# Kernel optimization log

Measured on AMD Instinct MI355X. Metric: run time of the kernel, lower is better.

Reference implementation:

```python
import jax, jax.numpy as jnp
import numpy as np

NHEAD = 8

def layernorm(x, w, b, eps=1e-5):
    mu = jnp.mean(x, axis=-1, keepdims=True)
    var = jnp.mean((x - mu) ** 2, axis=-1, keepdims=True)
    return (x - mu) * jax.lax.rsqrt(var + eps) * w + b

def setup_inputs() -> dict:
    key = jax.random.key(0)
    ks = jax.random.split(key, 3)
    N, in_dim, dim = 2048, 256, 256
    point = jax.random.normal(ks[0], (N, in_dim), dtype=jnp.float32)
    w_qkv = jax.random.normal(ks[1], (in_dim, 3 * dim), dtype=jnp.float32) * (in_dim ** -0.5)
    w_proj = jax.random.normal(ks[2], (dim, dim), dtype=jnp.float32) * (dim ** -0.5)
    return {
        "point": point,
        "w_qkv": w_qkv,
        "w_proj": w_proj,
        "b_proj": jnp.zeros((dim,), jnp.float32),
        "norm1_w": jnp.ones((in_dim,), jnp.float32),
        "norm1_b": jnp.zeros((in_dim,), jnp.float32),
        "norm2_w": jnp.ones((dim,), jnp.float32),
        "norm2_b": jnp.zeros((dim,), jnp.float32),
        "topk": 16,
    }

def reference(point, w_qkv, w_proj, b_proj, norm1_w, norm1_b, norm2_w, norm2_b, topk):
    # Coarse level of QTAttB (i == 0, ONE_BATCH=True)
    N, in_dim = point.shape
    dim = w_proj.shape[0]
    Ch = dim // NHEAD  # per-head channels
    x = layernorm(point, norm1_w, norm1_b)[None]            # [1, N, in_dim]
    qkv = (x @ w_qkv).reshape(1, N, 3, NHEAD, Ch)
    q, k, v = qkv[:, :, 0], qkv[:, :, 1], qkv[:, :, 2]      # [1, N, H, Ch]
    # QK: nlhd,nshd->nlsh ; softmax over key axis s (dim=-2 in torch = axis 2)
    QK = jnp.einsum('blhd,bshd->blsh', q, k)                # [1, N, N, H]
    A = jax.nn.softmax(QK * (Ch ** -0.5), axis=2)
    A_mean = jnp.mean(A, axis=-1)                           # [1, N, N]
    _, topk_idx = jax.lax.top_k(A_mean, topk)               # [1, N, topk]
    message = jnp.einsum('blsh,bshd->blhd', A, v).reshape(1, N, dim)
    message = message @ w_proj + b_proj
    message = v.reshape(1, N, dim) + message
    message = message[0]                                    # squeeze batch
    out = layernorm(message, norm2_w, norm2_b)              # final_message = norm2(message)
    return out, topk_idx[0]
```

## Files before the change

### kernel.cpp

```cpp
#include <hip/hip_runtime.h>

#define NTOK   2048
#define DIM    256
#define NH     8
#define CH     32
#define QB     8
#define TOPK_K 16
#define SCALE  0.17677669529663687f
#define LN_EPS 1e-5f

#define PBL    260
#define PBH    (QB * PBL)
#define PSCALE 16384.f
#define RPSCALE (1.f / 16384.f)

typedef _Float16 h16;
typedef _Float16 h16x8 __attribute__((ext_vector_type(8)));
typedef float    f32x4 __attribute__((ext_vector_type(4)));

#define MFMA16(a, b, c) __builtin_amdgcn_mfma_f32_16x16x32_f16((a), (b), (c), 0, 0, 0)


template<int NT>
__device__ __forceinline__ float block_sum(float v, float* red){
  #pragma unroll
  for (int off = 32; off > 0; off >>= 1) v += __shfl_xor(v, off, 64);
  const int t = threadIdx.x;
  if ((t & 63) == 0) red[t >> 6] = v;
  __syncthreads();
  float s = 0.f;
  #pragma unroll
  for (int w = 0; w < NT/64; w++) s += red[w];
  __syncthreads();
  return s;
}

__global__ __launch_bounds__(256) void reorder_w_kernel(
    const float* __restrict__ src_qkv, const float* __restrict__ src_proj,
    h16* __restrict__ WF, h16* __restrict__ WP)
{
  const int b = blockIdx.x;
  const float* src; h16* dst; int ld, pair;
  if (b < 96){ src = src_qkv;  dst = WF; ld = 768; pair = b * 4 + (threadIdx.x >> 6); }
  else       { src = src_proj; dst = WP; ld = 256; pair = (b - 96) * 4 + (threadIdx.x >> 6); }
  const int l  = threadIdx.x & 63;
  const int cg = pair >> 3, ks = pair & 7;
  h16x8 hi8, lo8;
  #pragma unroll
  for (int j = 0; j < 8; j++){
    const float v = src[(size_t)(ks * 32 + (l >> 4) * 8 + j) * ld + cg * 16 + (l & 15)];
    const h16 h = (h16)v;
    hi8[j] = h;
    lo8[j] = (h16)(v - (float)h);
  }
  *(h16x8*)&dst[(size_t)((cg * 8 + ks) * 2 + 0) * 512 + l * 8] = hi8;
  *(h16x8*)&dst[(size_t)((cg * 8 + ks) * 2 + 1) * 512 + l * 8] = lo8;
}

__global__ __launch_bounds__(1024) void ln_qkv_kernel(
    const float* __restrict__ point,
    const h16*   __restrict__ WF,
    const float* __restrict__ c1,
    const float* __restrict__ c2,
    float* __restrict__ Q,
    h16*   __restrict__ KF,
    h16*   __restrict__ VF,
    float* __restrict__ V)
{
  __shared__ float xs[16][261];
  __shared__ float garr[256], barr[256];
  __shared__ float red[16];
  const int t  = threadIdx.x;
  const int wv = t >> 6;
  const int l  = t & 63;
  const int r  = l & 15;
  const int g  = l >> 4;
  const int tg = blockIdx.x >> 1;
  const int ch = blockIdx.x & 1;
  const int l0 = tg * 16;

  const float a1 = (t < 256) ? c1[t] : 0.f;
  const float a2 = (t < 256) ? c2[t] : 0.f;
  const float s1 = block_sum<1024>(fabsf(a1), red);
  const float s2 = block_sum<1024>(fabsf(a2), red);
  if (t < 256){ garr[t] = (s1 > s2) ? a1 : a2; barr[t] = (s1 > s2) ? a2 : a1; }
  __syncthreads();

  {
    const float4 x = *(const float4*)&point[(size_t)(l0 + wv) * DIM + 4 * l];
    float s = x.x + x.y + x.z + x.w;
    #pragma unroll
    for (int off = 1; off < 64; off <<= 1) s += __shfl_xor(s, off, 64);
    const float mu = s * (1.f / DIM);
    const float d0 = x.x - mu, d1 = x.y - mu, d2 = x.z - mu, d3 = x.w - mu;
    float ss = d0 * d0 + d1 * d1 + d2 * d2 + d3 * d3;
    #pragma unroll
    for (int off = 1; off < 64; off <<= 1) ss += __shfl_xor(ss, off, 64);
    const float rsd = rsqrtf(ss * (1.f / DIM) + LN_EPS);
    xs[wv][4 * l + 0] = d0 * rsd * garr[4 * l + 0] + barr[4 * l + 0];
    xs[wv][4 * l + 1] = d1 * rsd * garr[4 * l + 1] + barr[4 * l + 1];
    xs[wv][4 * l + 2] = d2 * rsd * garr[4 * l + 2] + barr[4 * l + 2];
    xs[wv][4 * l + 3] = d3 * rsd * garr[4 * l + 3] + barr[4 * l + 3];
  }
  __syncthreads();

  h16x8 ah[8], al[8];
  #pragma unroll
  for (int ks = 0; ks < 8; ks++){
    #pragma unroll
    for (int j = 0; j < 8; j++){
      const float v = xs[r][ks * 32 + 8 * g + j];
      const h16 hi = (h16)v;
      ah[ks][j] = hi;
      al[ks][j] = (h16)(v - (float)hi);
    }
  }

  const int kgb = tg;
  #pragma unroll
  for (int cgi = 0; cgi < 2; cgi++){
    if (cgi == 1 && wv >= 8) break;
    const int cg = ch * 24 + (cgi == 0 ? wv : 16 + wv);
    f32x4 acc = {0.f, 0.f, 0.f, 0.f};
    const h16* wf = WF + (size_t)cg * 8192 + (size_t)l * 8;
    #pragma unroll
    for (int ks = 0; ks < 8; ks++){
      const h16x8 bh = *(const h16x8*)(wf + ks * 1024);
      const h16x8 bl = *(const h16x8*)(wf + ks * 1024 + 512);
      acc = MFMA16(ah[ks], bh, acc);
      acc = MFMA16(al[ks], bh, acc);
      acc = MFMA16(ah[ks], bl, acc);
    }
    const int typ = cg >> 4;
    const int c0  = (cg & 15) * 16 + r;
    #pragma unroll
    for (int q4 = 0; q4 < 4; q4++){
      const int tok = 4 * g + q4;
      if (typ == 0){
        Q[(size_t)(l0 + tok) * DIM + c0] = acc[q4];
      } else if (typ == 1){
        const int wh = c0 >> 5, gp = (c0 & 31) >> 3, jj = c0 & 7;
        const float kv = acc[q4];
        const h16 kh2 = (h16)kv;
        const size_t kidx = (size_t)(wh * 128 + kgb) * 1024
                          + (size_t)(gp * 16 + tok) * 8 + jj;
        KF[kidx]       = kh2;
        KF[kidx + 512] = (h16)(kv - (float)kh2);
      } else {
        V[(size_t)(l0 + tok) * DIM + c0] = acc[q4];
        const int wh = c0 >> 5, hh = (c0 & 31) >> 4, cp = c0 & 15;
        const int key = l0 + tok;
        const int kb = key >> 5, krem = key & 31, gpp = krem >> 3, jpp = krem & 7;
        VF[(size_t)((wh * 64 + kb) * 2 + hh) * 512
           + (size_t)(gpp * 16 + cp) * 8 + jpp] = (h16)acc[q4];
      }
    }
  }
}

__global__ __launch_bounds__(1024) void z_kernel(
    const float* __restrict__ Q,
    const h16*   __restrict__ KF,
    float*       __restrict__ Zp)
{
  const int t  = threadIdx.x;
  const int wv = t >> 6;
  const int w  = wv & 7;
  const int sh = wv >> 3;
  const int l  = t & 63;
  const int r  = l & 15;
  const int g  = l >> 4;
  const int tg = blockIdx.x >> 1;
  const int hb = blockIdx.x & 1;

  h16x8 qh, ql;
  {
    const float* qp = &Q[(size_t)(tg * 16 + r) * DIM + w * CH + 8 * g];
    const float4 q0 = *(const float4*)qp;
    const float4 q1 = *(const float4*)(qp + 4);
    const float qv[8] = {q0.x, q0.y, q0.z, q0.w, q1.x, q1.y, q1.z, q1.w};
    #pragma unroll
    for (int j = 0; j < 8; j++){
      const float s = qv[j] * SCALE;
      const h16 hi = (h16)s;
      qh[j] = hi;
      ql[j] = (h16)(s - (float)hi);
    }
  }

  const h16* kf = KF + (size_t)(w * 128 + hb * 64 + sh * 32) * 1024 + (size_t)l * 8;
  float zs[4] = {0.f, 0.f, 0.f, 0.f};
  #pragma unroll 2
  for (int kgi = 0; kgi < 32; kgi++){
    const h16x8 bh = *(const h16x8*)(kf + (size_t)kgi * 1024);
    const h16x8 bl = *(const h16x8*)(kf + (size_t)kgi * 1024 + 512);
    f32x4 d = {0.f, 0.f, 0.f, 0.f};
    d = MFMA16(qh, bh, d);
    d = MFMA16(ql, bh, d);
    d = MFMA16(qh, bl, d);
    #pragma unroll
    for (int q4 = 0; q4 < 4; q4++) zs[q4] += __expf(d[q4]);
  }
  #pragma unroll
  for (int q4 = 0; q4 < 4; q4++){
    #pragma unroll
    for (int off = 1; off < 16; off <<= 1) zs[q4] += __shfl_xor(zs[q4], off, 64);
  }
  if (r == 0){
    #pragma unroll
    for (int q4 = 0; q4 < 4; q4++)
      Zp[(size_t)((hb * 2 + sh) * NH + w) * NTOK + tg * 16 + 4 * g + q4] = zs[q4];
  }
}

__global__ __launch_bounds__(1024) __attribute__((amdgpu_waves_per_eu(4)))
void attn_fused_kernel(
    const float* Q,
    const h16*   __restrict__ KF,
    const h16*   __restrict__ VF,
    const float* __restrict__ Zp,
    float*       msg,
    float*       __restrict__ out_idx)
{
  __shared__ float pbuf[NH * PBH];
  __shared__ float am[QB][NTOK];
  __shared__ float msg_s[2][QB][DIM + 4];
  __shared__ float zbuf[NH * QB];

  const int t  = threadIdx.x;
  const int wv = t >> 6;
  const int w  = wv & 7;
  const int hf = wv >> 3;
  const int l  = t & 63;
  const int r  = l & 15;
  const int g  = l >> 4;
  const int l0 = blockIdx.x * QB;

  h16x8 qh, ql;
  #pragma unroll
  for (int j = 0; j < 8; j++){ qh[j] = (h16)0.f; ql[j] = (h16)0.f; }
  if (r < QB){
    const float* qp = &Q[(size_t)(l0 + r) * DIM + w * CH + 8 * g];
    const float4 q0 = *(const float4*)qp;
    const float4 q1 = *(const float4*)(qp + 4);
    const float qv[8] = {q0.x, q0.y, q0.z, q0.w, q1.x, q1.y, q1.z, q1.w};
    #pragma unroll
    for (int j = 0; j < 8; j++){
      const float s = qv[j] * SCALE;
      const h16 hi = (h16)s;
      qh[j] = hi;
      ql[j] = (h16)(s - (float)hi);
    }
  }

  if (t < 64){
    const int h = t >> 3, q = t & 7;
    float z = 0.f;
    #pragma unroll
    for (int p = 0; p < 4; p++) z += Zp[(size_t)(p * NH + h) * NTOK + l0 + q];
    zbuf[t] = z;
  }
  __syncthreads();
  float rZ[4];
  #pragma unroll
  for (int q4 = 0; q4 < 4; q4++){
    const int row = 4 * g + q4;
    rZ[q4] = (g < 2) ? 1.f / zbuf[w * QB + row] : 0.f;
  }

  const h16* kfw = KF + (size_t)(w * 128) * 1024 + (size_t)l * 8;
  const h16* vfw = VF + (size_t)(w * 64) * 1024 + (size_t)l * 8;

  f32x4 macc[2];
  #pragma unroll
  for (int dg = 0; dg < 2; dg++) macc[dg] = (f32x4){0.f, 0.f, 0.f, 0.f};

  for (int ti = 0; ti < 8; ti++){
    const int s0 = ti * 256;
    const h16* vft = vfw + (size_t)((ti * 8 + hf * 4) * 2) * 512;

    h16x8 pva[4], pvb[4];
    pva[0] = *(const h16x8*)(vft);
    pvb[0] = *(const h16x8*)(vft + 512);
    pva[1] = *(const h16x8*)(vft + 1024);
    pvb[1] = *(const h16x8*)(vft + 1024 + 512);

    {
      const h16* kft = kfw + (size_t)(ti * 16 + hf * 8) * 1024;
      #pragma unroll 2
      for (int kgi = 0; kgi < 8; kgi++){
        const h16x8 bh = *(const h16x8*)(kft + (size_t)kgi * 1024);
        const h16x8 bl = *(const h16x8*)(kft + (size_t)kgi * 1024 + 512);
        f32x4 d = {0.f, 0.f, 0.f, 0.f};
        d = MFMA16(qh, bh, d);
        d = MFMA16(ql, bh, d);
        d = MFMA16(qh, bl, d);
        if (g < 2){
          const int kbr = hf * 128 + kgi * 16 + r;
          pbuf[w * PBH + (4 * g + 0) * PBL + kbr] = __expf(d[0]) * rZ[0];
          pbuf[w * PBH + (4 * g + 1) * PBL + kbr] = __expf(d[1]) * rZ[1];
          pbuf[w * PBH + (4 * g + 2) * PBL + kbr] = __expf(d[2]) * rZ[2];
          pbuf[w * PBH + (4 * g + 3) * PBL + kbr] = __expf(d[3]) * rZ[3];
        }
      }
    }
    __syncthreads();

    pva[2] = *(const h16x8*)(vft + 2048);
    pvb[2] = *(const h16x8*)(vft + 2048 + 512);
    pva[3] = *(const h16x8*)(vft + 3072);
    pvb[3] = *(const h16x8*)(vft + 3072 + 512);

    #pragma unroll
    for (int st = 0; st < 4; st++){
      h16x8 pa;
      #pragma unroll
      for (int j = 0; j < 8; j++) pa[j] = (h16)0.f;
      if (r < QB){
        const float* pp = &pbuf[w * PBH + r * PBL + hf * 128 + st * 32 + 8 * g];
        const float4 p0 = *(const float4*)pp;
        const float4 p1 = *(const float4*)(pp + 4);
        pa[0] = (h16)(p0.x * PSCALE); pa[1] = (h16)(p0.y * PSCALE);
        pa[2] = (h16)(p0.z * PSCALE); pa[3] = (h16)(p0.w * PSCALE);
        pa[4] = (h16)(p1.x * PSCALE); pa[5] = (h16)(p1.y * PSCALE);
        pa[6] = (h16)(p1.z * PSCALE); pa[7] = (h16)(p1.w * PSCALE);
      }
      macc[0] = MFMA16(pa, pva[st], macc[0]);
      macc[1] = MFMA16(pa, pvb[st], macc[1]);
    }
    if (t < 512){
      const int q = t >> 6, k4 = (t & 63) * 4;
      float4 su = make_float4(0.f, 0.f, 0.f, 0.f);
      #pragma unroll
      for (int hh = 0; hh < 8; hh++){
        const float4 v = *(const float4*)&pbuf[hh * PBH + q * PBL + k4];
        su.x += v.x; su.y += v.y; su.z += v.z; su.w += v.w;
      }
      *(float4*)&am[q][s0 + k4] =
          make_float4(su.x * 0.125f, su.y * 0.125f, su.z * 0.125f, su.w * 0.125f);
    }
    __syncthreads();
  }

  if (g < 2){
    #pragma unroll
    for (int dg = 0; dg < 2; dg++)
      #pragma unroll
      for (int q4 = 0; q4 < 4; q4++)
        msg_s[hf][4 * g + q4][w * CH + dg * 16 + r] = macc[dg][q4] * RPSCALE;
  }
  __syncthreads();

  if (wv < QB){
    for (int it = 0; it < TOPK_K; it++){
      float bv = -1e30f; int bi = 0x7fffffff;
      #pragma unroll
      for (int b = 0; b < NTOK / 64; b++){
        const int idx = b * 64 + l;
        const float v = am[wv][idx];
        if (v > bv || (v == bv && idx < bi)){ bv = v; bi = idx; }
      }
      #pragma unroll
      for (int off = 1; off < 64; off <<= 1){
        const float ov = __shfl_xor(bv, off, 64);
        const int   oi = __shfl_xor(bi, off, 64);
        if (ov > bv || (ov == bv && oi < bi)){ bv = ov; bi = oi; }
      }
      if (l == 0){
        out_idx[(l0 + wv) * TOPK_K + it] = (float)bi;
        am[wv][bi] = -1e30f;
      }
    }
  } else {
    const int t2 = t - 512;
    #pragma unroll
    for (int k2 = 0; k2 < 4; k2++){
      const int cell = t2 + 512 * k2;
      const int q = cell >> 8, dcol = cell & 255;
      msg[(size_t)(l0 + q) * DIM + dcol] = msg_s[0][q][dcol] + msg_s[1][q][dcol];
    }
  }
}

__global__ __launch_bounds__(1024) void proj_ln_kernel(
    const float* __restrict__ msg,
    const float* __restrict__ V,
    const h16*   __restrict__ WP,
    const float* __restrict__ b_proj,
    const float* __restrict__ c1,
    const float* __restrict__ c2,
    float* __restrict__ out)
{
  __shared__ float xs[16][261];
  __shared__ float ms2[16][261];
  __shared__ float garr[256], barr[256], bparr[256];
  __shared__ float red[16];
  const int t  = threadIdx.x;
  const int wv = t >> 6;
  const int l  = t & 63;
  const int r  = l & 15;
  const int g  = l >> 4;
  const int l0 = blockIdx.x * 16;

  const float a1 = (t < 256) ? c1[t] : 0.f;
  const float a2 = (t < 256) ? c2[t] : 0.f;
  const float s1 = block_sum<1024>(fabsf(a1), red);
  const float s2 = block_sum<1024>(fabsf(a2), red);
  if (t < 256){
    garr[t]  = (s1 > s2) ? a1 : a2;
    barr[t]  = (s1 > s2) ? a2 : a1;
    bparr[t] = b_proj[t];
  }

  {
    const float4 x = *(const float4*)&msg[(size_t)(l0 + wv) * DIM + 4 * l];
    xs[wv][4 * l + 0] = x.x; xs[wv][4 * l + 1] = x.y;
    xs[wv][4 * l + 2] = x.z; xs[wv][4 * l + 3] = x.w;
  }
  __syncthreads();

  h16x8 ah[8], al[8];
  #pragma unroll
  for (int ks = 0; ks < 8; ks++){
    #pragma unroll
    for (int j = 0; j < 8; j++){
      const float v = xs[r][ks * 32 + 8 * g + j];
      const h16 hi = (h16)v;
      ah[ks][j] = hi;
      al[ks][j] = (h16)(v - (float)hi);
    }
  }

  f32x4 acc = {0.f, 0.f, 0.f, 0.f};
  {
    const h16* wp = WP + (size_t)wv * 8192 + (size_t)l * 8;
    #pragma unroll
    for (int ks = 0; ks < 8; ks++){
      const h16x8 bh = *(const h16x8*)(wp + ks * 1024);
      const h16x8 bl = *(const h16x8*)(wp + ks * 1024 + 512);
      acc = MFMA16(ah[ks], bh, acc);
      acc = MFMA16(al[ks], bh, acc);
      acc = MFMA16(ah[ks], bl, acc);
    }
  }

  const int dc = wv * 16 + r;
  #pragma unroll
  for (int q4 = 0; q4 < 4; q4++){
    const int tok = 4 * g + q4;
    ms2[tok][dc] = acc[q4] + bparr[dc] + V[(size_t)(l0 + tok) * DIM + dc];
  }
  __syncthreads();

  {
    const float x0 = ms2[wv][4 * l + 0], x1 = ms2[wv][4 * l + 1];
    const float x2 = ms2[wv][4 * l + 2], x3 = ms2[wv][4 * l + 3];
    float s = x0 + x1 + x2 + x3;
    #pragma unroll
    for (int off = 1; off < 64; off <<= 1) s += __shfl_xor(s, off, 64);
    const float mu = s * (1.f / DIM);
    const float d0 = x0 - mu, d1 = x1 - mu, d2 = x2 - mu, d3 = x3 - mu;
    float ss = d0 * d0 + d1 * d1 + d2 * d2 + d3 * d3;
    #pragma unroll
    for (int off = 1; off < 64; off <<= 1) ss += __shfl_xor(ss, off, 64);
    const float rsd = rsqrtf(ss * (1.f / DIM) + LN_EPS);
    float4 o;
    o.x = d0 * rsd * garr[4 * l + 0] + barr[4 * l + 0];
    o.y = d1 * rsd * garr[4 * l + 1] + barr[4 * l + 1];
    o.z = d2 * rsd * garr[4 * l + 2] + barr[4 * l + 2];
    o.w = d3 * rsd * garr[4 * l + 3] + barr[4 * l + 3];
    *(float4*)&out[(size_t)(l0 + wv) * DIM + 4 * l] = o;
  }
}

extern "C" void kernel_launch(void* const* d_in, const int* in_sizes, int n_in,
                              void* d_out, int out_size, void* d_ws, size_t ws_size,
                              hipStream_t stream) {
  const float* point  = nullptr;
  const float* w_qkv  = nullptr;
  const float* w_proj = nullptr;
  const float* v256[5] = {nullptr, nullptr, nullptr, nullptr, nullptr};
  int n256 = 0;
  for (int i = 0; i < n_in; i++){
    const int sz = in_sizes[i];
    if      (sz == NTOK * DIM)      point  = (const float*)d_in[i];
    else if (sz == DIM * 3 * DIM)   w_qkv  = (const float*)d_in[i];
    else if (sz == DIM * DIM)       w_proj = (const float*)d_in[i];
    else if (sz == DIM && n256 < 5) v256[n256++] = (const float*)d_in[i];
  }
  const float* b_proj = v256[0];
  const float* n1a    = v256[1];
  const float* n1c    = v256[2];
  const float* n2a    = v256[3];
  const float* n2c    = v256[4];

  float* out     = (float*)d_out;
  float* out_idx = out + (size_t)NTOK * DIM;

  char* ws = (char*)d_ws;
  float* Q   = (float*)(ws);
  float* V   = (float*)(ws + ((size_t)2 << 20));
  h16*   KF  = (h16*)  (ws + ((size_t)4 << 20));
  h16*   VF  = (h16*)  (ws + ((size_t)6 << 20));
  h16*   WF  = (h16*)  (ws + ((size_t)7 << 20));
  h16*   WP  = (h16*)  (ws + ((size_t)7 << 20) + 786432);
  float* msg = Q;
  float* Zp  = out;

  reorder_w_kernel <<<128,       256,  0, stream>>>(w_qkv, w_proj, WF, WP);
  ln_qkv_kernel    <<<256,       1024, 0, stream>>>(point, WF, n1a, n1c, Q, KF, VF, V);
  z_kernel         <<<256,       1024, 0, stream>>>(Q, KF, Zp);
  attn_fused_kernel<<<NTOK / QB, 1024, 0, stream>>>(Q, KF, VF, Zp, msg, out_idx);
  proj_ln_kernel   <<<NTOK / 16, 1024, 0, stream>>>(msg, V, WP, b_proj, n2a, n2c, out);
}
```

Before: 181.0 us.

## Split attention keys across two blocks with full 16-row query tiles and two-stage top-k

The query tile grows from 8 to 16 rows, so the MFMA rows that were previously zero-padded now do real work. Each block handles one half of the keys. Partial messages are combined with atomicAdd into the output buffer, and each half writes 16 top-k candidates that a new topk_kernel merges. Q is stored once as prescaled fp16 hi/lo fragments instead of being converted from fp32 in both the z and attention kernels. The z partial sums are now accumulated with atomics too. This adds a zeroing kernel, an extra launch, atomic traffic and a reuse of workspace buffers.

```diff
diff --git a/kernel.cpp b/kernel.cpp
--- a/kernel.cpp
+++ b/kernel.cpp
@@ -4,7 +4,7 @@
 #define DIM    256
 #define NH     8
 #define CH     32
-#define QB     8
+#define QB     16
 #define TOPK_K 16
 #define SCALE  0.17677669529663687f
 #define LN_EPS 1e-5f
@@ -57,12 +57,20 @@
   *(h16x8*)&dst[(size_t)((cg * 8 + ks) * 2 + 1) * 512 + l * 8] = lo8;
 }
 
+__global__ __launch_bounds__(256) void zero2_kernel(
+    float* __restrict__ a, int na, float* __restrict__ b, int nb)
+{
+  const int stride = gridDim.x * blockDim.x;
+  for (int k = blockIdx.x * blockDim.x + threadIdx.x; k < na; k += stride) a[k] = 0.f;
+  for (int k = blockIdx.x * blockDim.x + threadIdx.x; k < nb; k += stride) b[k] = 0.f;
+}
+
 __global__ __launch_bounds__(1024) void ln_qkv_kernel(
     const float* __restrict__ point,
     const h16*   __restrict__ WF,
     const float* __restrict__ c1,
     const float* __restrict__ c2,
-    float* __restrict__ Q,
+    h16*   __restrict__ QF,
     h16*   __restrict__ KF,
     h16*   __restrict__ VF,
     float* __restrict__ V)
@@ -137,7 +145,12 @@
     for (int q4 = 0; q4 < 4; q4++){
       const int tok = 4 * g + q4;
       if (typ == 0){
-        Q[(size_t)(l0 + tok) * DIM + c0] = acc[q4];
+        const float qs = acc[q4] * SCALE;
+        const h16 qhi = (h16)qs;
+        const int wq = c0 >> 5, gq = (c0 & 31) >> 3, jq = c0 & 7;
+        const size_t qidx = (((size_t)(tg * 8 + wq) * 2 + 0) * 64 + (gq * 16 + tok)) * 8 + jq;
+        QF[qidx]       = qhi;
+        QF[qidx + 512] = (h16)(qs - (float)qhi);
       } else if (typ == 1){
         const int wh = c0 >> 5, gp = (c0 & 31) >> 3, jj = c0 & 7;
         const float kv = acc[q4];
@@ -159,9 +172,9 @@
 }
 
 __global__ __launch_bounds__(1024) void z_kernel(
-    const float* __restrict__ Q,
-    const h16*   __restrict__ KF,
-    float*       __restrict__ Zp)
+    const h16* __restrict__ QF,
+    const h16* __restrict__ KF,
+    float*     __restrict__ Zp)
 {
   const int t  = threadIdx.x;
   const int wv = t >> 6;
@@ -173,20 +186,9 @@
   const int tg = blockIdx.x >> 1;
   const int hb = blockIdx.x & 1;
 
-  h16x8 qh, ql;
-  {
-    const float* qp = &Q[(size_t)(tg * 16 + r) * DIM + w * CH + 8 * g];
-    const float4 q0 = *(const float4*)qp;
-    const float4 q1 = *(const float4*)(qp + 4);
-    const float qv[8] = {q0.x, q0.y, q0.z, q0.w, q1.x, q1.y, q1.z, q1.w};
-    #pragma unroll
-    for (int j = 0; j < 8; j++){
-      const float s = qv[j] * SCALE;
-      const h16 hi = (h16)s;
-      qh[j] = hi;
-      ql[j] = (h16)(s - (float)hi);
-    }
-  }
+  const h16* qf = QF + ((size_t)(tg * 8 + w) * 2) * 512 + (size_t)l * 8;
+  const h16x8 qh = *(const h16x8*)(qf);
+  const h16x8 ql = *(const h16x8*)(qf + 512);
 
   const h16* kf = KF + (size_t)(w * 128 + hb * 64 + sh * 32) * 1024 + (size_t)l * 8;
   float zs[4] = {0.f, 0.f, 0.f, 0.f};
@@ -209,23 +211,23 @@
   if (r == 0){
     #pragma unroll
     for (int q4 = 0; q4 < 4; q4++)
-      Zp[(size_t)((hb * 2 + sh) * NH + w) * NTOK + tg * 16 + 4 * g + q4] = zs[q4];
+      atomicAdd(&Zp[(size_t)w * NTOK + tg * 16 + 4 * g + q4], zs[q4]);
   }
 }
 
 __global__ __launch_bounds__(1024) __attribute__((amdgpu_waves_per_eu(4)))
 void attn_fused_kernel(
-    const float* Q,
+    const h16*   __restrict__ QF,
     const h16*   __restrict__ KF,
     const h16*   __restrict__ VF,
     const float* __restrict__ Zp,
-    float*       msg,
-    float*       __restrict__ out_idx)
+    float*       __restrict__ msgacc,
+    float2*      __restrict__ candG)
 {
   __shared__ float pbuf[NH * PBH];
-  __shared__ float am[QB][NTOK];
-  __shared__ float msg_s[2][QB][DIM + 4];
-  __shared__ float zbuf[NH * QB];
+  __shared__ float cand_v[16][64];
+  __shared__ float cand_i[16][64];
+  __shared__ float zbuf[NH][QB];
 
   const int t  = threadIdx.x;
   const int wv = t >> 6;
@@ -234,49 +236,28 @@
   const int l  = t & 63;
   const int r  = l & 15;
   const int g  = l >> 4;
-  const int l0 = blockIdx.x * QB;
-
-  h16x8 qh, ql;
-  #pragma unroll
-  for (int j = 0; j < 8; j++){ qh[j] = (h16)0.f; ql[j] = (h16)0.f; }
-  if (r < QB){
-    const float* qp = &Q[(size_t)(l0 + r) * DIM + w * CH + 8 * g];
-    const float4 q0 = *(const float4*)qp;
-    const float4 q1 = *(const float4*)(qp + 4);
-    const float qv[8] = {q0.x, q0.y, q0.z, q0.w, q1.x, q1.y, q1.z, q1.w};
-    #pragma unroll
-    for (int j = 0; j < 8; j++){
-      const float s = qv[j] * SCALE;
-      const h16 hi = (h16)s;
-      qh[j] = hi;
-      ql[j] = (h16)(s - (float)hi);
-    }
-  }
-
-  if (t < 64){
-    const int h = t >> 3, q = t & 7;
-    float z = 0.f;
-    #pragma unroll
-    for (int p = 0; p < 4; p++) z += Zp[(size_t)(p * NH + h) * NTOK + l0 + q];
-    zbuf[t] = z;
-  }
+  const int qt = blockIdx.x >> 1;
+  const int hb = blockIdx.x & 1;
+  const int l0 = qt * 16;
+
+  const h16* qf = QF + ((size_t)(qt * 8 + w) * 2) * 512 + (size_t)l * 8;
+  const h16x8 qh = *(const h16x8*)(qf);
+  const h16x8 ql = *(const h16x8*)(qf + 512);
+
+  if (t < 128) zbuf[t >> 4][t & 15] = Zp[(size_t)(t >> 4) * NTOK + l0 + (t & 15)];
   __syncthreads();
   float rZ[4];
   #pragma unroll
-  for (int q4 = 0; q4 < 4; q4++){
-    const int row = 4 * g + q4;
-    rZ[q4] = (g < 2) ? 1.f / zbuf[w * QB + row] : 0.f;
-  }
-
-  const h16* kfw = KF + (size_t)(w * 128) * 1024 + (size_t)l * 8;
-  const h16* vfw = VF + (size_t)(w * 64) * 1024 + (size_t)l * 8;
+  for (int q4 = 0; q4 < 4; q4++) rZ[q4] = 1.f / zbuf[w][4 * g + q4];
+
+  const h16* kfw = KF + (size_t)(w * 128 + hb * 64) * 1024 + (size_t)l * 8;
+  const h16* vfw = VF + (size_t)(w * 64 + hb * 32) * 1024 + (size_t)l * 8;
 
   f32x4 macc[2];
   #pragma unroll
   for (int dg = 0; dg < 2; dg++) macc[dg] = (f32x4){0.f, 0.f, 0.f, 0.f};
 
-  for (int ti = 0; ti < 8; ti++){
-    const int s0 = ti * 256;
+  for (int ti = 0; ti < 4; ti++){
     const h16* vft = vfw + (size_t)((ti * 8 + hf * 4) * 2) * 512;
 
     h16x8 pva[4], pvb[4];
@@ -295,13 +276,11 @@
         d = MFMA16(qh, bh, d);
         d = MFMA16(ql, bh, d);
         d = MFMA16(qh, bl, d);
-        if (g < 2){
-          const int kbr = hf * 128 + kgi * 16 + r;
-          pbuf[w * PBH + (4 * g + 0) * PBL + kbr] = __expf(d[0]) * rZ[0];
-          pbuf[w * PBH + (4 * g + 1) * PBL + kbr] = __expf(d[1]) * rZ[1];
-          pbuf[w * PBH + (4 * g + 2) * PBL + kbr] = __expf(d[2]) * rZ[2];
-          pbuf[w * PBH + (4 * g + 3) * PBL + kbr] = __expf(d[3]) * rZ[3];
-        }
+        const int kbr = hf * 128 + kgi * 16 + r;
+        pbuf[w * PBH + (4 * g + 0) * PBL + kbr] = __expf(d[0]) * rZ[0];
+        pbuf[w * PBH + (4 * g + 1) * PBL + kbr] = __expf(d[1]) * rZ[1];
+        pbuf[w * PBH + (4 * g + 2) * PBL + kbr] = __expf(d[2]) * rZ[2];
+        pbuf[w * PBH + (4 * g + 3) * PBL + kbr] = __expf(d[3]) * rZ[3];
       }
     }
     __syncthreads();
@@ -314,71 +293,110 @@
     #pragma unroll
     for (int st = 0; st < 4; st++){
       h16x8 pa;
-      #pragma unroll
-      for (int j = 0; j < 8; j++) pa[j] = (h16)0.f;
-      if (r < QB){
-        const float* pp = &pbuf[w * PBH + r * PBL + hf * 128 + st * 32 + 8 * g];
-        const float4 p0 = *(const float4*)pp;
-        const float4 p1 = *(const float4*)(pp + 4);
-        pa[0] = (h16)(p0.x * PSCALE); pa[1] = (h16)(p0.y * PSCALE);
-        pa[2] = (h16)(p0.z * PSCALE); pa[3] = (h16)(p0.w * PSCALE);
-        pa[4] = (h16)(p1.x * PSCALE); pa[5] = (h16)(p1.y * PSCALE);
-        pa[6] = (h16)(p1.z * PSCALE); pa[7] = (h16)(p1.w * PSCALE);
-      }
+      const float* pp = &pbuf[w * PBH + r * PBL + hf * 128 + st * 32 + 8 * g];
+      const float4 p0 = *(const float4*)pp;
+      const float4 p1 = *(const float4*)(pp + 4);
+      pa[0] = (h16)(p0.x * PSCALE); pa[1] = (h16)(p0.y * PSCALE);
+      pa[2] = (h16)(p0.z * PSCALE); pa[3] = (h16)(p0.w * PSCALE);
+      pa[4] = (h16)(p1.x * PSCALE); pa[5] = (h16)(p1.y * PSCALE);
+      pa[6] = (h16)(p1.z * PSCALE); pa[7] = (h16)(p1.w * PSCALE);
       macc[0] = MFMA16(pa, pva[st], macc[0]);
       macc[1] = MFMA16(pa, pvb[st], macc[1]);
     }
-    if (t < 512){
-      const int q = t >> 6, k4 = (t & 63) * 4;
+
+    {
       float4 su = make_float4(0.f, 0.f, 0.f, 0.f);
       #pragma unroll
       for (int hh = 0; hh < 8; hh++){
-        const float4 v = *(const float4*)&pbuf[hh * PBH + q * PBL + k4];
+        const float4 v = *(const float4*)&pbuf[hh * PBH + wv * PBL + 4 * l];
         su.x += v.x; su.y += v.y; su.z += v.z; su.w += v.w;
       }
-      *(float4*)&am[q][s0 + k4] =
-          make_float4(su.x * 0.125f, su.y * 0.125f, su.z * 0.125f, su.w * 0.125f);
+      float v0 = su.x * 0.125f, v1 = su.y * 0.125f;
+      float v2 = su.z * 0.125f, v3 = su.w * 0.125f;
+      const int base = hb * 1024 + ti * 256 + 4 * l;
+      #pragma unroll
+      for (int it = 0; it < 16; it++){
+        float bv = v0; int bj = 0;
+        if (v1 > bv){ bv = v1; bj = 1; }
+        if (v2 > bv){ bv = v2; bj = 2; }
+        if (v3 > bv){ bv = v3; bj = 3; }
+        int bi = base + bj;
+        #pragma unroll
+        for (int off = 1; off < 64; off <<= 1){
+          const float ov = __shfl_xor(bv, off, 64);
+          const int   oi = __shfl_xor(bi, off, 64);
+          if (ov > bv || (ov == bv && oi < bi)){ bv = ov; bi = oi; }
+        }
+        if (l == 0){ cand_v[wv][ti * 16 + it] = bv; cand_i[wv][ti * 16 + it] = (float)bi; }
+        const int dj = bi - base;
+        if (dj >= 0 && dj < 4){
+          if      (dj == 0) v0 = -1e30f;
+          else if (dj == 1) v1 = -1e30f;
+          else if (dj == 2) v2 = -1e30f;
+          else              v3 = -1e30f;
+        }
+      }
     }
     __syncthreads();
   }
 
-  if (g < 2){
-    #pragma unroll
-    for (int dg = 0; dg < 2; dg++)
-      #pragma unroll
-      for (int q4 = 0; q4 < 4; q4++)
-        msg_s[hf][4 * g + q4][w * CH + dg * 16 + r] = macc[dg][q4] * RPSCALE;
-  }
-  __syncthreads();
-
-  if (wv < QB){
-    for (int it = 0; it < TOPK_K; it++){
-      float bv = -1e30f; int bi = 0x7fffffff;
-      #pragma unroll
-      for (int b = 0; b < NTOK / 64; b++){
-        const int idx = b * 64 + l;
-        const float v = am[wv][idx];
-        if (v > bv || (v == bv && idx < bi)){ bv = v; bi = idx; }
-      }
+  {
+    float mv = cand_v[wv][l];
+    float mi = cand_i[wv][l];
+    #pragma unroll
+    for (int it = 0; it < 16; it++){
+      float bv = mv, bi = mi;
       #pragma unroll
       for (int off = 1; off < 64; off <<= 1){
         const float ov = __shfl_xor(bv, off, 64);
-        const int   oi = __shfl_xor(bi, off, 64);
+        const float oi = __shfl_xor(bi, off, 64);
         if (ov > bv || (ov == bv && oi < bi)){ bv = ov; bi = oi; }
       }
       if (l == 0){
-        out_idx[(l0 + wv) * TOPK_K + it] = (float)bi;
-        am[wv][bi] = -1e30f;
+        float2 c; c.x = bv; c.y = bi;
+        candG[((size_t)(l0 + wv) * 2 + hb) * 16 + it] = c;
       }
-    }
-  } else {
-    const int t2 = t - 512;
-    #pragma unroll
-    for (int k2 = 0; k2 < 4; k2++){
-      const int cell = t2 + 512 * k2;
-      const int q = cell >> 8, dcol = cell & 255;
-      msg[(size_t)(l0 + q) * DIM + dcol] = msg_s[0][q][dcol] + msg_s[1][q][dcol];
-    }
+      if (mi == bi) mv = -1e30f;
+    }
+  }
+
+  float* msg_s = pbuf;
+  #pragma unroll
+  for (int dg = 0; dg < 2; dg++)
+    #pragma unroll
+    for (int q4 = 0; q4 < 4; q4++)
+      msg_s[(hf * 16 + 4 * g + q4) * PBL + w * CH + dg * 16 + r] = macc[dg][q4] * RPSCALE;
+  __syncthreads();
+  #pragma unroll
+  for (int k2 = 0; k2 < 4; k2++){
+    const int cell = t + 1024 * k2;
+    const int q = cell >> 8, d = cell & 255;
+    const float val = msg_s[(q) * PBL + d] + msg_s[(16 + q) * PBL + d];
+    atomicAdd(&msgacc[(size_t)(l0 + q) * DIM + d], val);
+  }
+}
+
+__global__ __launch_bounds__(1024) void topk_kernel(
+    const float2* __restrict__ candG, float* __restrict__ out_idx)
+{
+  const int wv = threadIdx.x >> 6, l = threadIdx.x & 63;
+  const int row = blockIdx.x * 16 + wv;
+  float v = -1e30f, fi = 1e9f;
+  if (l < 32){
+    const float2 p = candG[(size_t)row * 32 + l];
+    v = p.x; fi = p.y;
+  }
+  #pragma unroll
+  for (int it = 0; it < TOPK_K; it++){
+    float bv = v, bi = fi;
+    #pragma unroll
+    for (int off = 1; off < 64; off <<= 1){
+      const float ov = __shfl_xor(bv, off, 64);
+      const float oi = __shfl_xor(bi, off, 64);
+      if (ov > bv || (ov == bv && oi < bi)){ bv = ov; bi = oi; }
+    }
+    if (l == 0) out_idx[(size_t)row * TOPK_K + it] = bi;
+    if (fi == bi) v = -1e30f;
   }
 }
 
@@ -498,18 +516,21 @@
   float* out_idx = out + (size_t)NTOK * DIM;
 
   char* ws = (char*)d_ws;
-  float* Q   = (float*)(ws);
+  h16*   QF  = (h16*)  (ws);
   float* V   = (float*)(ws + ((size_t)2 << 20));
   h16*   KF  = (h16*)  (ws + ((size_t)4 << 20));
   h16*   VF  = (h16*)  (ws + ((size_t)6 << 20));
   h16*   WF  = (h16*)  (ws + ((size_t)7 << 20));
   h16*   WP  = (h16*)  (ws + ((size_t)7 << 20) + 786432);
-  float* msg = Q;
-  float* Zp  = out;
-
-  reorder_w_kernel <<<128,       256,  0, stream>>>(w_qkv, w_proj, WF, WP);
-  ln_qkv_kernel    <<<256,       1024, 0, stream>>>(point, WF, n1a, n1c, Q, KF, VF, V);
-  z_kernel         <<<256,       1024, 0, stream>>>(Q, KF, Zp);
-  attn_fused_kernel<<<NTOK / QB, 1024, 0, stream>>>(Q, KF, VF, Zp, msg, out_idx);
-  proj_ln_kernel   <<<NTOK / 16, 1024, 0, stream>>>(msg, V, WP, b_proj, n2a, n2c, out);
-}
+  float2* candG = (float2*)(ws + ((size_t)7 << 20));
+  float*  Zp    = (float*) (ws + ((size_t)7 << 20) + 524288);
+  float*  msgacc = out;
+
+  reorder_w_kernel <<<128, 256,  0, stream>>>(w_qkv, w_proj, WF, WP);
+  ln_qkv_kernel    <<<256, 1024, 0, stream>>>(point, WF, n1a, n1c, QF, KF, VF, V);
+  zero2_kernel     <<<512, 256,  0, stream>>>(msgacc, NTOK * DIM, Zp, NH * NTOK);
+  z_kernel         <<<256, 1024, 0, stream>>>(QF, KF, Zp);
+  attn_fused_kernel<<<256, 1024, 0, stream>>>(QF, KF, VF, Zp, msgacc, candG);
+  topk_kernel      <<<128, 1024, 0, stream>>>(candG, out_idx);
+  proj_ln_kernel   <<<128, 1024, 0, stream>>>(msgacc, V, WP, b_proj, n2a, n2c, out);
+}
```

Measured after the change: 198.6 us. 1.1x slower.
